# Performance work log

Hardware: AMD Instinct MI355X
Metric: run time of the kernel (lower is better)

Reference implementation:

```python
import jax, jax.numpy as jnp
import numpy as np

B, D, H = 64, 512, 8
EPS = 1e-8


def setup_inputs() -> dict:
    key = jax.random.key(0)
    k1, k2, k3 = jax.random.split(key, 3)
    x = jax.random.normal(k1, (B, D), dtype=jnp.float32)
    # alphas/betas: one scalar per (head, transform); columns = (query, key, value)
    alphas = jax.random.uniform(k2, (H, 3), dtype=jnp.float32)
    betas = jax.random.uniform(k3, (H, 3), dtype=jnp.float32)
    return {"x": x, "alphas": alphas, "betas": betas}


def reference(x, alphas, betas):
    # x: [B, D]; alphas, betas: [H, 3] (query, key, value scalar affine params per head)
    d = x.shape[-1]
    # qkv[h, t, b, d] = alphas[h, t] * x[b, d] + betas[h, t]  (ones vector -> plain bias)
    qkv = alphas[:, :, None, None] * x[None, None, :, :] + betas[:, :, None, None]  # [H,3,B,D]
    q, k, v = qkv[:, 0], qkv[:, 1], qkv[:, 2]  # each [H, B, D]
    # diff[h,b,i,j] = |q[h,b,j] - k[h,b,i]|  (row i = key feature, col j = query feature)
    diff = jnp.abs(q[:, :, None, :] - k[:, :, :, None]) + EPS  # [H, B, D, D]
    sim = jax.nn.softmax(1.0 / diff, axis=-1) / jnp.sqrt(jnp.float32(d))
    # attended[h,b,i] = sum_j sim[h,b,i,j] * v[h,b,j]  (batched matvec)
    attended = jnp.einsum("hbij,hbj->hbi", sim, v)  # [H, B, D]
    return x + attended.sum(axis=0)
```

## Files before the change

kernel.cpp:

```cpp
#include <hip/hip_runtime.h>
#include <math.h>

#define BB 64
#define DD 512
#define HH 8
#define EPS 1e-8f

__device__ __forceinline__ float fast_rcp(float d) {
    return __builtin_amdgcn_rcpf(d);
}

__global__ __launch_bounds__(512, 8) void flattn_kernel(
    const float* __restrict__ x,
    const float* __restrict__ alphas,
    const float* __restrict__ betas,
    float* __restrict__ out)
{
    const int b  = blockIdx.x;
    const int ic = blockIdx.y;
    const int h  = blockIdx.z;

    __shared__ float xs[DD];
    __shared__ float mind_sh[2][256];
    __shared__ float ss_sh[256];
    __shared__ float sx_sh[256];

    const int tid = threadIdx.x;
    const int ii  = tid & 255;
    const int jc  = tid >> 8;
    const int i   = ic * 256 + ii;

    const float a0 = alphas[h * 3 + 0];
    const float a1 = alphas[h * 3 + 1];
    const float a2 = alphas[h * 3 + 2];
    const float b0 = betas[h * 3 + 0];
    const float b1 = betas[h * 3 + 1];
    const float b2 = betas[h * 3 + 2];

    xs[tid] = x[b * DD + tid];
    __syncthreads();

    const float xi = xs[i];
    const float c  = b0 - fmaf(a1, xi, b1);

    const int j0 = jc * 256;

    float mind = 3.0e38f;
    #pragma unroll 4
    for (int j = j0; j < j0 + 256; j += 4) {
        float4 x4 = *(const float4*)&xs[j];
        mind = fminf(mind, fabsf(fmaf(a0, x4.x, c)));
        mind = fminf(mind, fabsf(fmaf(a0, x4.y, c)));
        mind = fminf(mind, fabsf(fmaf(a0, x4.z, c)));
        mind = fminf(mind, fabsf(fmaf(a0, x4.w, c)));
    }
    mind_sh[jc][ii] = mind;
    __syncthreads();

    mind = fminf(mind_sh[0][ii], mind_sh[1][ii]);
    const float m = fast_rcp(mind + EPS);
    const float log2e = 1.4426950408889634f;
    const float negml = -m * log2e;

    float ss = 0.0f, sx = 0.0f;
    #pragma unroll 2
    for (int j = j0; j < j0 + 256; j += 4) {
        float4 x4 = *(const float4*)&xs[j];
        {
            float t = fmaf(a0, x4.x, c);
            float r = fast_rcp(fabsf(t) + EPS);
            float s = __builtin_amdgcn_exp2f(fmaf(r, log2e, negml));
            ss += s; sx = fmaf(s, x4.x, sx);
        }
        {
            float t = fmaf(a0, x4.y, c);
            float r = fast_rcp(fabsf(t) + EPS);
            float s = __builtin_amdgcn_exp2f(fmaf(r, log2e, negml));
            ss += s; sx = fmaf(s, x4.y, sx);
        }
        {
            float t = fmaf(a0, x4.z, c);
            float r = fast_rcp(fabsf(t) + EPS);
            float s = __builtin_amdgcn_exp2f(fmaf(r, log2e, negml));
            ss += s; sx = fmaf(s, x4.z, sx);
        }
        {
            float t = fmaf(a0, x4.w, c);
            float r = fast_rcp(fabsf(t) + EPS);
            float s = __builtin_amdgcn_exp2f(fmaf(r, log2e, negml));
            ss += s; sx = fmaf(s, x4.w, sx);
        }
    }

    if (jc == 1) { ss_sh[ii] = ss; sx_sh[ii] = sx; }
    __syncthreads();
    if (jc == 0) {
        ss += ss_sh[ii];
        sx += sx_sh[ii];
        const float scale = 0.04419417382415922f;
        float sv  = fmaf(a2, sx, b2 * ss);
        float att = sv * fast_rcp(ss) * scale;
        if (h == 0) att += xi;
        atomicAdd(&out[b * DD + i], att);
    }
}

extern "C" void kernel_launch(void* const* d_in, const int* in_sizes, int n_in,
                              void* d_out, int out_size, void* d_ws, size_t ws_size,
                              hipStream_t stream) {
    const float* x      = (const float*)d_in[0];
    const float* alphas = (const float*)d_in[1];
    const float* betas  = (const float*)d_in[2];
    float* out = (float*)d_out;

    hipMemsetAsync(out, 0, (size_t)out_size * sizeof(float), stream);

    dim3 grid(BB, 2, HH);
    dim3 block(512);
    flattn_kernel<<<grid, block, 0, stream>>>(x, alphas, betas, out);
}
```

Before: 90.73 us.

## Sort inputs per batch and restrict softmax to a narrow window of dominant keys

```diff
diff --git a/kernel.cpp b/kernel.cpp
--- a/kernel.cpp
+++ b/kernel.cpp
@@ -6,8 +6,40 @@
 #define HH 8
 #define EPS 1e-8f
 
+__device__ float g_xsorted[BB][DD];
+__device__ int   g_perm[BB][DD];
+
 __device__ __forceinline__ float fast_rcp(float d) {
     return __builtin_amdgcn_rcpf(d);
+}
+
+__global__ __launch_bounds__(DD) void sort_kernel(const float* __restrict__ x)
+{
+    const int b   = blockIdx.x;
+    const int tid = threadIdx.x;
+    __shared__ float sv[DD];
+    __shared__ int   si[DD];
+    sv[tid] = x[b * DD + tid];
+    si[tid] = tid;
+    __syncthreads();
+    for (int k = 2; k <= DD; k <<= 1) {
+        for (int j = k >> 1; j > 0; j >>= 1) {
+            const int ixj = tid ^ j;
+            if (ixj > tid) {
+                const bool up = ((tid & k) == 0);
+                float v0 = sv[tid], v1 = sv[ixj];
+                bool sw = up ? (v0 > v1) : (v0 < v1);
+                if (sw) {
+                    int i0 = si[tid], i1 = si[ixj];
+                    sv[tid] = v1; sv[ixj] = v0;
+                    si[tid] = i1; si[ixj] = i0;
+                }
+            }
+            __syncthreads();
+        }
+    }
+    g_xsorted[b][tid] = sv[tid];
+    g_perm[b][tid]    = si[tid];
 }
 
 __global__ __launch_bounds__(512, 8) void flattn_kernel(
@@ -21,14 +53,15 @@
     const int h  = blockIdx.z;
 
     __shared__ float xs[DD];
+    __shared__ float xss[DD];
     __shared__ float mind_sh[2][256];
     __shared__ float ss_sh[256];
     __shared__ float sx_sh[256];
 
-    const int tid = threadIdx.x;
-    const int ii  = tid & 255;
-    const int jc  = tid >> 8;
-    const int i   = ic * 256 + ii;
+    const int tid  = threadIdx.x;
+    const int ii   = tid & 255;
+    const int jc   = tid >> 8;
+    const int rank = ic * 256 + ii;
 
     const float a0 = alphas[h * 3 + 0];
     const float a1 = alphas[h * 3 + 1];
@@ -37,58 +70,118 @@
     const float b1 = betas[h * 3 + 1];
     const float b2 = betas[h * 3 + 2];
 
-    xs[tid] = x[b * DD + tid];
-    __syncthreads();
-
-    const float xi = xs[i];
+    xs[tid]  = x[b * DD + tid];
+    xss[tid] = g_xsorted[b][tid];
+    __syncthreads();
+
+    const float xi = xss[rank];
     const float c  = b0 - fmaf(a1, xi, b1);
 
+    const float ra0 = fast_rcp(a0);
+    const float u   = -c * ra0;
+
+    int pos = 0;
+    #pragma unroll
+    for (int s = 512; s > 0; s >>= 1) {
+        int p = pos + s;
+        float v = xss[(p <= 512 ? p : 512) - 1];
+        pos = (p <= 512 && v < u) ? p : pos;
+    }
+    float mind_hat = 3.0e38f;
+    #pragma unroll
+    for (int q = -2; q <= 1; ++q) {
+        int cidx = pos + q;
+        if (cidx >= 0 && cidx < DD)
+            mind_hat = fminf(mind_hat, fabsf(fmaf(a0, xss[cidx], c)));
+    }
+    const float mhat = fast_rcp(mind_hat + EPS);
+
+    const float th  = fast_rcp(fmaxf(mhat - 30.0f, 1e-30f));
+    const float tha = fmaf(th * 1.0001f, ra0, 1e-6f);
+    const float xlo = u - tha;
+    const float xhi = u + tha;
+
+    int lo = 0, hi = 0;
+    #pragma unroll
+    for (int s = 512; s > 0; s >>= 1) {
+        int pl = lo + s, ph = hi + s;
+        float vl = xss[(pl <= 512 ? pl : 512) - 1];
+        float vh = xss[(ph <= 512 ? ph : 512) - 1];
+        lo = (pl <= 512 && vl <  xlo) ? pl : lo;
+        hi = (ph <= 512 && vh <= xhi) ? ph : hi;
+    }
+    lo = max(lo - 2, 0);
+    hi = min(hi + 2, DD);
+    const int len = hi - lo;
+
+    const bool lane_peaked = (a0 > 1e-6f) && (mhat > 60.0f) && (len <= 64);
+    const bool peaked = __all(lane_peaked);
+
+    const float log2e = 1.4426950408889634f;
+
+    float md = 3.0e38f;
+    int wl = 0, wh = 0;
     const int j0 = jc * 256;
-
-    float mind = 3.0e38f;
-    #pragma unroll 4
-    for (int j = j0; j < j0 + 256; j += 4) {
-        float4 x4 = *(const float4*)&xs[j];
-        mind = fminf(mind, fabsf(fmaf(a0, x4.x, c)));
-        mind = fminf(mind, fabsf(fmaf(a0, x4.y, c)));
-        mind = fminf(mind, fabsf(fmaf(a0, x4.z, c)));
-        mind = fminf(mind, fabsf(fmaf(a0, x4.w, c)));
-    }
-    mind_sh[jc][ii] = mind;
-    __syncthreads();
-
-    mind = fminf(mind_sh[0][ii], mind_sh[1][ii]);
-    const float m = fast_rcp(mind + EPS);
-    const float log2e = 1.4426950408889634f;
+    if (peaked) {
+        const int mid = lo + ((len + 1) >> 1);
+        wl = jc ? mid : lo;
+        wh = jc ? hi  : mid;
+        for (int k = wl; k < wh; ++k)
+            md = fminf(md, fabsf(fmaf(a0, xss[k], c)));
+    } else {
+        #pragma unroll 4
+        for (int j = j0; j < j0 + 256; j += 4) {
+            float4 x4 = *(const float4*)&xs[j];
+            md = fminf(md, fabsf(fmaf(a0, x4.x, c)));
+            md = fminf(md, fabsf(fmaf(a0, x4.y, c)));
+            md = fminf(md, fabsf(fmaf(a0, x4.z, c)));
+            md = fminf(md, fabsf(fmaf(a0, x4.w, c)));
+        }
+    }
+    mind_sh[jc][ii] = md;
+    __syncthreads();
+
+    const float mind  = fminf(mind_sh[0][ii], mind_sh[1][ii]);
+    const float m     = fast_rcp(mind + EPS);
     const float negml = -m * log2e;
 
     float ss = 0.0f, sx = 0.0f;
-    #pragma unroll 2
-    for (int j = j0; j < j0 + 256; j += 4) {
-        float4 x4 = *(const float4*)&xs[j];
-        {
-            float t = fmaf(a0, x4.x, c);
-            float r = fast_rcp(fabsf(t) + EPS);
-            float s = __builtin_amdgcn_exp2f(fmaf(r, log2e, negml));
-            ss += s; sx = fmaf(s, x4.x, sx);
-        }
-        {
-            float t = fmaf(a0, x4.y, c);
-            float r = fast_rcp(fabsf(t) + EPS);
-            float s = __builtin_amdgcn_exp2f(fmaf(r, log2e, negml));
-            ss += s; sx = fmaf(s, x4.y, sx);
-        }
-        {
-            float t = fmaf(a0, x4.z, c);
-            float r = fast_rcp(fabsf(t) + EPS);
-            float s = __builtin_amdgcn_exp2f(fmaf(r, log2e, negml));
-            ss += s; sx = fmaf(s, x4.z, sx);
-        }
-        {
-            float t = fmaf(a0, x4.w, c);
-            float r = fast_rcp(fabsf(t) + EPS);
-            float s = __builtin_amdgcn_exp2f(fmaf(r, log2e, negml));
-            ss += s; sx = fmaf(s, x4.w, sx);
+    if (peaked) {
+        for (int k = wl; k < wh; ++k) {
+            float xv = xss[k];
+            float t  = fmaf(a0, xv, c);
+            float r  = fast_rcp(fabsf(t) + EPS);
+            float s  = __builtin_amdgcn_exp2f(fmaf(r, log2e, negml));
+            ss += s; sx = fmaf(s, xv, sx);
+        }
+    } else {
+        #pragma unroll 2
+        for (int j = j0; j < j0 + 256; j += 4) {
+            float4 x4 = *(const float4*)&xs[j];
+            {
+                float t = fmaf(a0, x4.x, c);
+                float r = fast_rcp(fabsf(t) + EPS);
+                float s = __builtin_amdgcn_exp2f(fmaf(r, log2e, negml));
+                ss += s; sx = fmaf(s, x4.x, sx);
+            }
+            {
+                float t = fmaf(a0, x4.y, c);
+                float r = fast_rcp(fabsf(t) + EPS);
+                float s = __builtin_amdgcn_exp2f(fmaf(r, log2e, negml));
+                ss += s; sx = fmaf(s, x4.y, sx);
+            }
+            {
+                float t = fmaf(a0, x4.z, c);
+                float r = fast_rcp(fabsf(t) + EPS);
+                float s = __builtin_amdgcn_exp2f(fmaf(r, log2e, negml));
+                ss += s; sx = fmaf(s, x4.z, sx);
+            }
+            {
+                float t = fmaf(a0, x4.w, c);
+                float r = fast_rcp(fabsf(t) + EPS);
+                float s = __builtin_amdgcn_exp2f(fmaf(r, log2e, negml));
+                ss += s; sx = fmaf(s, x4.w, sx);
+            }
         }
     }
 
@@ -101,7 +194,8 @@
         float sv  = fmaf(a2, sx, b2 * ss);
         float att = sv * fast_rcp(ss) * scale;
         if (h == 0) att += xi;
-        atomicAdd(&out[b * DD + i], att);
+        const int i_orig = g_perm[b][rank];
+        atomicAdd(&out[b * DD + i_orig], att);
     }
 }
 
@@ -115,6 +209,8 @@
 
     hipMemsetAsync(out, 0, (size_t)out_size * sizeof(float), stream);
 
+    sort_kernel<<<dim3(BB), dim3(DD), 0, stream>>>(x);
+
     dim3 grid(BB, 2, HH);
     dim3 block(512);
     flattn_kernel<<<grid, block, 0, stream>>>(x, alphas, betas, out);
```

Measured after the change: 98.69 us. 8.8% more time.
